# Performance work log

Hardware: AMD Instinct MI355X
Metric: run time of the kernel (lower is better)

Reference implementation:

```python
import jax, jax.numpy as jnp
import numpy as np

N = 50000
E = 800000
IN_C, HID_C, OUT_C = 256, 128, 64


def setup_inputs() -> dict:
    key = jax.random.key(0)
    k1, k2, k3, k4 = jax.random.split(key, 4)
    x = jax.random.normal(k1, (N, IN_C), dtype=jnp.float32)
    edge_index = jax.random.randint(k2, (2, E), 0, N, dtype=jnp.int64)
    # Glorot-ish init for GCN weights, zero bias (PyG default)
    W1 = jax.random.normal(k3, (IN_C, HID_C), dtype=jnp.float32) / np.sqrt(IN_C)
    b1 = jnp.zeros((HID_C,), dtype=jnp.float32)
    W2 = jax.random.normal(k4, (HID_C, OUT_C), dtype=jnp.float32) / np.sqrt(HID_C)
    b2 = jnp.zeros((OUT_C,), dtype=jnp.float32)
    return {"x": x, "edge_index": edge_index, "W1": W1, "b1": b1, "W2": W2, "b2": b2}


def _gcn_norm(edge_index, num_nodes):
    # Add self-loops, compute symmetric normalization D^-1/2 A D^-1/2 (PyG GCNConv default)
    loops = jnp.arange(num_nodes, dtype=edge_index.dtype)
    src = jnp.concatenate([edge_index[0], loops])  # message sources
    dst = jnp.concatenate([edge_index[1], loops])  # aggregation targets
    deg = jax.ops.segment_sum(jnp.ones_like(dst, dtype=jnp.float32), dst,
                              num_segments=num_nodes)
    dinv = jnp.where(deg > 0, jax.lax.rsqrt(deg), 0.0)
    norm = dinv[src] * dinv[dst]  # [E+N]
    return src, dst, norm


def _gcn_conv(x, W, b, src, dst, norm, num_nodes):
    h = x @ W                                   # [N, out]
    msg = h[src] * norm[:, None]                # gather + scale, [E+N, out]
    out = jax.ops.segment_sum(msg, dst, num_segments=num_nodes)  # scatter-add
    return out + b


def reference(x, edge_index, W1, b1, W2, b2):
    num_nodes = x.shape[0]
    src, dst, norm = _gcn_norm(edge_index, num_nodes)
    h = _gcn_conv(x, W1, b1, src, dst, norm, num_nodes)
    h = jax.nn.relu(h)
    # F.dropout(training=False) -> identity at inference
    return _gcn_conv(h, W2, b2, src, dst, norm, num_nodes)
```

## Files before the change

### kernel.cpp

```cpp
#include <hip/hip_runtime.h>
#include <hip/hip_bf16.h>


typedef __attribute__((ext_vector_type(8))) short short8;
typedef __attribute__((ext_vector_type(4))) float f32x4;

union BF8 {
    short8 s;
    uint4 u;
    __hip_bfloat162 h[4];
};

__device__ __forceinline__ unsigned short f32_to_bf16_rne(float f) {
    unsigned u = __float_as_uint(f);
    return (unsigned short)((u + 0x7fffu + ((u >> 16) & 1u)) >> 16);
}
__device__ __forceinline__ float bf_lo(unsigned v) { return __uint_as_float(v << 16); }
__device__ __forceinline__ float bf_hi(unsigned v) { return __uint_as_float(v & 0xffff0000u); }

__global__ void count_deg_kernel(const int* __restrict__ dst, int* __restrict__ counts, int e) {
    int i = blockIdx.x * blockDim.x + threadIdx.x;
    if (i < e) atomicAdd(&counts[dst[i]], 1);
}

__global__ void wfrag_zero_kernel(const float* __restrict__ W1, const float* __restrict__ W2,
                                  unsigned short* __restrict__ w1f,
                                  unsigned short* __restrict__ w2f,
                                  int* __restrict__ counts, int n) {
    int i = blockIdx.x * blockDim.x + threadIdx.x;
    if (i < n) counts[i] = 0;
    const float* W;
    unsigned short* WF;
    int KS, NCOL, idx;
    if (i < 32768) {
        W = W1; WF = w1f; KS = 8; NCOL = 128; idx = i;
    } else if (i < 32768 + 8192) {
        W = W2; WF = w2f; KS = 4; NCOL = 64; idx = i - 32768;
    } else return;
    int j = idx & 7;
    int lane = (idx >> 3) & 63;
    int f = idx >> 9;
    int ks = f % KS, nt = f / KS;
    int m16 = lane & 15, quad = lane >> 4;
    int ncol = nt * 16 + m16;
    int k = ks * 32 + quad * 8 + j;
    WF[idx] = f32_to_bf16_rne(W[k * NCOL + ncol]);
}

__global__ __launch_bounds__(256) void scan_partial_kernel(const int* __restrict__ counts,
                                                           int* __restrict__ bsums,
                                                           float* __restrict__ dinv, int n) {
    __shared__ int wsum[4];
    const int tid = threadIdx.x;
    const int lane = tid & 63, wv = tid >> 6;
    int base = blockIdx.x * 1024 + tid * 4;
    int s = 0;
#pragma unroll
    for (int j = 0; j < 4; j++) {
        int i = base + j;
        if (i < n) {
            int c = counts[i];
            s += c;
            dinv[i] = rsqrtf((float)c + 1.0f);
        }
    }
#pragma unroll
    for (int off = 1; off < 64; off <<= 1) {
        int y = __shfl_up(s, off, 64);
        if (lane >= off) s += y;
    }
    if (lane == 63) wsum[wv] = s;
    __syncthreads();
    if (tid == 0) bsums[blockIdx.x] = wsum[0] + wsum[1] + wsum[2] + wsum[3];
}

__global__ __launch_bounds__(256) void scan_final_kernel(const int* __restrict__ counts,
                                                         const int* __restrict__ bsums,
                                                         int* __restrict__ rowptr,
                                                         int* __restrict__ bcursor,
                                                         int n, int nb) {
    __shared__ int wsum[4];
    __shared__ int blockOff;
    const int tid = threadIdx.x;
    const int lane = tid & 63, wv = tid >> 6;
    if (tid < 64) {
        int v = (tid < nb) ? bsums[tid] : 0;
        int x = v;
#pragma unroll
        for (int off = 1; off < 64; off <<= 1) {
            int y = __shfl_up(x, off, 64);
            if (lane >= off) x += y;
        }
        int pref = (blockIdx.x == 0) ? 0 : __shfl(x, blockIdx.x - 1, 64);
        if (tid == 0) blockOff = pref;
    }
    int base = blockIdx.x * 1024 + tid * 4;
    int v[4];
#pragma unroll
    for (int j = 0; j < 4; j++) {
        int i = base + j;
        v[j] = (i < n) ? counts[i] : 0;
    }
    int tot = v[0] + v[1] + v[2] + v[3];
    int x = tot;
#pragma unroll
    for (int off = 1; off < 64; off <<= 1) {
        int y = __shfl_up(x, off, 64);
        if (lane >= off) x += y;
    }
    if (lane == 63) wsum[wv] = x;
    __syncthreads();
    int wpre = 0;
    for (int k = 0; k < wv; k++) wpre += wsum[k];
    int pre = blockOff + wpre + (x - tot);
#pragma unroll
    for (int j = 0; j < 4; j++) {
        int i = base + j;
        if (i <= n) rowptr[i] = pre;
        if (i < n && (i & 255) == 0) bcursor[i >> 8] = pre;
        pre += v[j];
    }
}

#define ACHUNK 2048
__global__ __launch_bounds__(256) void bucketA_kernel(const int* __restrict__ src,
                                                      const int* __restrict__ dst,
                                                      int* __restrict__ bcursor,
                                                      int2* __restrict__ tmp, int e, int nb) {
    __shared__ int sdst[ACHUNK];
    __shared__ int hist[256];
    const int tid = threadIdx.x;
    const int start = blockIdx.x * ACHUNK;
    const int cnt = min(ACHUNK, e - start);
    if (tid < nb) hist[tid] = 0;
    __syncthreads();
    for (int i = tid; i < cnt; i += 256) {
        int d = dst[start + i];
        sdst[i] = d;
        atomicAdd(&hist[d >> 8], 1);
    }
    __syncthreads();
    if (tid < nb) {
        int h = hist[tid];
        hist[tid] = (h > 0) ? atomicAdd(&bcursor[tid], h) : 0;
    }
    __syncthreads();
    for (int i = tid; i < cnt; i += 256) {
        int d = sdst[i];
        int slot = atomicAdd(&hist[d >> 8], 1);
        tmp[slot] = make_int2(src[start + i], d);
    }
}

__global__ __launch_bounds__(256) void bucketB_kernel(const int* __restrict__ rowptr,
                                                      const int2* __restrict__ tmp,
                                                      const float* __restrict__ dinv,
                                                      int2* __restrict__ sedge, int n) {
    __shared__ int lcur[256];
    __shared__ float ldinv[256];
    const int tid = threadIdx.x;
    const int nodeBase = blockIdx.x * 256;
    const int nNodes = min(256, n - nodeBase);
    if (tid < nNodes) {
        lcur[tid] = rowptr[nodeBase + tid];
        ldinv[tid] = dinv[nodeBase + tid];
    }
    __syncthreads();
    const int beg = rowptr[nodeBase];
    const int end = rowptr[nodeBase + nNodes];
    for (int i = beg + tid; i < end; i += 256) {
        int2 r = tmp[i];
        int j = r.y - nodeBase;
        float w = dinv[r.x] * ldinv[j];
        int pos = atomicAdd(&lcur[j], 1);
        sedge[pos] = make_int2(r.x, __float_as_int(w));
    }
}

__global__ __launch_bounds__(256) void agg128_kernel(
    const int* __restrict__ rowptr, const int2* __restrict__ sedge,
    const unsigned short* __restrict__ hb, const float* __restrict__ dinv,
    const float* __restrict__ bias, unsigned short* __restrict__ outb, int n) {
    int node = blockIdx.x * 8 + (threadIdx.x >> 5);
    if (node >= n) return;
    int sub = threadIdx.x & 31;
    float di = dinv[node];
    float d2 = di * di;
    uint2 sv = ((const uint2*)(hb + (size_t)node * 128))[sub];
    float a0 = d2 * bf_lo(sv.x), a1 = d2 * bf_hi(sv.x);
    float a2 = d2 * bf_lo(sv.y), a3 = d2 * bf_hi(sv.y);
    int beg = rowptr[node], end = rowptr[node + 1];
    int i = beg;
    for (; i + 8 <= end; i += 8) {
        int2 e[8];
        uint2 v[8];
#pragma unroll
        for (int j = 0; j < 8; j++) e[j] = sedge[i + j];
#pragma unroll
        for (int j = 0; j < 8; j++)
            v[j] = ((const uint2*)(hb + (size_t)e[j].x * 128))[sub];
#pragma unroll
        for (int j = 0; j < 8; j++) {
            float w = __int_as_float(e[j].y);
            a0 = fmaf(w, bf_lo(v[j].x), a0);
            a1 = fmaf(w, bf_hi(v[j].x), a1);
            a2 = fmaf(w, bf_lo(v[j].y), a2);
            a3 = fmaf(w, bf_hi(v[j].y), a3);
        }
    }
    for (; i + 4 <= end; i += 4) {
        int2 e[4];
        uint2 v[4];
#pragma unroll
        for (int j = 0; j < 4; j++) e[j] = sedge[i + j];
#pragma unroll
        for (int j = 0; j < 4; j++)
            v[j] = ((const uint2*)(hb + (size_t)e[j].x * 128))[sub];
#pragma unroll
        for (int j = 0; j < 4; j++) {
            float w = __int_as_float(e[j].y);
            a0 = fmaf(w, bf_lo(v[j].x), a0);
            a1 = fmaf(w, bf_hi(v[j].x), a1);
            a2 = fmaf(w, bf_lo(v[j].y), a2);
            a3 = fmaf(w, bf_hi(v[j].y), a3);
        }
    }
    for (; i < end; ++i) {
        int2 e = sedge[i];
        float w = __int_as_float(e.y);
        uint2 v = ((const uint2*)(hb + (size_t)e.x * 128))[sub];
        a0 = fmaf(w, bf_lo(v.x), a0);
        a1 = fmaf(w, bf_hi(v.x), a1);
        a2 = fmaf(w, bf_lo(v.y), a2);
        a3 = fmaf(w, bf_hi(v.y), a3);
    }
    float4 bv = ((const float4*)bias)[sub];
    float r0 = fmaxf(a0 + bv.x, 0.0f);
    float r1 = fmaxf(a1 + bv.y, 0.0f);
    float r2 = fmaxf(a2 + bv.z, 0.0f);
    float r3 = fmaxf(a3 + bv.w, 0.0f);
    BF8 p;
    p.h[0] = __float22bfloat162_rn(make_float2(r0, r1));
    p.h[1] = __float22bfloat162_rn(make_float2(r2, r3));
    ((uint2*)(outb + (size_t)node * 128))[sub] = make_uint2(p.u.x, p.u.y);
}

__global__ __launch_bounds__(256) void agg64_kernel(
    const int* __restrict__ rowptr, const int2* __restrict__ sedge,
    const unsigned short* __restrict__ hb, const float* __restrict__ dinv,
    const float* __restrict__ bias, float* __restrict__ out, int n) {
    int node = blockIdx.x * 8 + (threadIdx.x >> 5);
    if (node >= n) return;
    int sub = threadIdx.x & 31;
    float di = dinv[node];
    float d2 = di * di;
    unsigned sv = ((const unsigned*)(hb + (size_t)node * 64))[sub];
    float ax = d2 * bf_lo(sv), ay = d2 * bf_hi(sv);
    int beg = rowptr[node], end = rowptr[node + 1];
    int i = beg;
    for (; i + 8 <= end; i += 8) {
        int2 e[8];
        unsigned v[8];
#pragma unroll
        for (int j = 0; j < 8; j++) e[j] = sedge[i + j];
#pragma unroll
        for (int j = 0; j < 8; j++)
            v[j] = ((const unsigned*)(hb + (size_t)e[j].x * 64))[sub];
#pragma unroll
        for (int j = 0; j < 8; j++) {
            float w = __int_as_float(e[j].y);
            ax = fmaf(w, bf_lo(v[j]), ax);
            ay = fmaf(w, bf_hi(v[j]), ay);
        }
    }
    for (; i + 4 <= end; i += 4) {
        int2 e[4];
        unsigned v[4];
#pragma unroll
        for (int j = 0; j < 4; j++) e[j] = sedge[i + j];
#pragma unroll
        for (int j = 0; j < 4; j++)
            v[j] = ((const unsigned*)(hb + (size_t)e[j].x * 64))[sub];
#pragma unroll
        for (int j = 0; j < 4; j++) {
            float w = __int_as_float(e[j].y);
            ax = fmaf(w, bf_lo(v[j]), ax);
            ay = fmaf(w, bf_hi(v[j]), ay);
        }
    }
    for (; i < end; ++i) {
        int2 e = sedge[i];
        float w = __int_as_float(e.y);
        unsigned v = ((const unsigned*)(hb + (size_t)e.x * 64))[sub];
        ax = fmaf(w, bf_lo(v), ax);
        ay = fmaf(w, bf_hi(v), ay);
    }
    float2 bv = ((const float2*)bias)[sub];
    ((float2*)(out + (size_t)node * 64))[sub] = make_float2(ax + bv.x, ay + bv.y);
}

template <int NT, int KS, bool BFA>
__global__ __launch_bounds__(256) void mfma_gemm_kernel(
    const void* __restrict__ Av, const unsigned short* __restrict__ BFRAG,
    unsigned short* __restrict__ C, int M) {
    constexpr int NCOL = NT * 16;
    constexpr int K = KS * 32;
    constexpr int LSTRIDE = K + 8;
    __shared__ unsigned short Alds[64 * LSTRIDE];

    const int tid = threadIdx.x;
    const int wave = tid >> 6, lane = tid & 63;
    const int quad = lane >> 4, m16 = lane & 15;
    const int rowBase = blockIdx.x * 64;

    if constexpr (BFA) {
        const unsigned short* Ab = (const unsigned short*)Av;
        constexpr int ITERS = K / 32;
        uint4 v[ITERS];
#pragma unroll
        for (int it = 0; it < ITERS; it++) {
            int p = it * 2048 + tid * 8;
            int rg = rowBase + p / K;
            if (rg >= M) rg = M - 1;
            v[it] = *(const uint4*)(Ab + (size_t)rg * K + (p % K));
        }
#pragma unroll
        for (int it = 0; it < ITERS; it++) {
            int p = it * 2048 + tid * 8;
            *(uint4*)&Alds[(p / K) * LSTRIDE + (p % K)] = v[it];
        }
    } else {
        const float* Af = (const float*)Av;
        constexpr int HALVES = K / 128;
#pragma unroll
        for (int h = 0; h < HALVES; h++) {
            f32x4 v[8];
#pragma unroll
            for (int it = 0; it < 8; it++) {
                int p = (h * 8 + it) * 1024 + tid * 4;
                int rg = rowBase + p / K;
                if (rg >= M) rg = M - 1;
                v[it] = *(const f32x4*)(Af + (size_t)rg * K + (p % K));
            }
#pragma unroll
            for (int it = 0; it < 8; it++) {
                int p = (h * 8 + it) * 1024 + tid * 4;
                BF8 cv;
                cv.h[0] = __float22bfloat162_rn(make_float2(v[it].x, v[it].y));
                cv.h[1] = __float22bfloat162_rn(make_float2(v[it].z, v[it].w));
                *(uint2*)&Alds[(p / K) * LSTRIDE + (p % K)] = make_uint2(cv.u.x, cv.u.y);
            }
        }
    }
    __syncthreads();

    const unsigned short* Afrag0 = &Alds[(wave * 16 + m16) * LSTRIDE + quad * 8];
    const uint4* Bfrag = (const uint4*)BFRAG + lane;

    f32x4 acc[NT];
#pragma unroll
    for (int nt = 0; nt < NT; nt++) acc[nt] = f32x4{0.f, 0.f, 0.f, 0.f};

#pragma unroll
    for (int ks = 0; ks < KS; ks++) {
        BF8 af;
        af.u = *(const uint4*)(Afrag0 + ks * 32);
#pragma unroll
        for (int nt = 0; nt < NT; nt++) {
            BF8 bf;
            bf.u = Bfrag[(nt * KS + ks) * 64];
            acc[nt] = __builtin_amdgcn_mfma_f32_16x16x32_bf16(af.s, bf.s, acc[nt], 0, 0, 0);
        }
    }

    const int rowOut = rowBase + wave * 16 + quad * 4;
#pragma unroll
    for (int nt = 0; nt < NT; nt++) {
#pragma unroll
        for (int r = 0; r < 4; r++) {
            int row = rowOut + r;
            if (row < M)
                C[(size_t)row * NCOL + nt * 16 + m16] = f32_to_bf16_rne(acc[nt][r]);
        }
    }
}

extern "C" void kernel_launch(void* const* d_in, const int* in_sizes, int n_in,
                              void* d_out, int out_size, void* d_ws, size_t ws_size,
                              hipStream_t stream) {
    const float* x  = (const float*)d_in[0];
    const int*   ei = (const int*)d_in[1];
    const float* W1 = (const float*)d_in[2];
    const float* b1 = (const float*)d_in[3];
    const float* W2 = (const float*)d_in[4];
    const float* b2 = (const float*)d_in[5];
    float* out = (float*)d_out;

    const int IN_C = 256;
    const int N = in_sizes[0] / IN_C;
    const int E = in_sizes[1] / 2;
    const int* srcA = ei;
    const int* dstA = ei + E;

    char* ws = (char*)d_ws;
    const size_t KB = 1024, MB = 1024 * 1024;
    int*            counts  = (int*)(ws);
    float*          dinv    = (float*)(ws + 256 * KB);
    int*            rowptr  = (int*)(ws + 512 * KB);
    int*            bcursor = (int*)(ws + 768 * KB);
    int*            bsums   = (int*)(ws + 992 * KB);
    unsigned short* w1f     = (unsigned short*)(ws + 1 * MB);
    unsigned short* w2f     = (unsigned short*)(ws + 1 * MB + 64 * KB);
    int2*           sedge   = (int2*)(ws + 2 * MB);
    int2*           tmp     = (int2*)(ws + 9 * MB);
    unsigned short* h1b     = (unsigned short*)(ws + 16 * MB);
    unsigned short* a1b     = (unsigned short*)(ws + 29 * MB);
    unsigned short* h2b     = h1b;

    const int eb256 = (E + 255) / 256;
    const int nbScan = (N + 1 + 1023) / 1024;
    const int NB = (N + 255) / 256;
    const int gGemm = (N + 63) / 64;
    const int gWfrag = (max(N, 32768 + 8192) + 255) / 256;

    wfrag_zero_kernel<<<gWfrag, 256, 0, stream>>>(W1, W2, w1f, w2f, counts, N);
    count_deg_kernel<<<eb256, 256, 0, stream>>>(dstA, counts, E);
    scan_partial_kernel<<<nbScan, 256, 0, stream>>>(counts, bsums, dinv, N);
    scan_final_kernel<<<nbScan, 256, 0, stream>>>(counts, bsums, rowptr, bcursor, N, nbScan);
    bucketA_kernel<<<(E + ACHUNK - 1) / ACHUNK, 256, 0, stream>>>(srcA, dstA, bcursor, tmp, E, NB);
    bucketB_kernel<<<NB, 256, 0, stream>>>(rowptr, tmp, dinv, sedge, N);

    mfma_gemm_kernel<8, 8, false><<<gGemm, 256, 0, stream>>>(x, w1f, h1b, N);
    agg128_kernel<<<(N + 7) / 8, 256, 0, stream>>>(rowptr, sedge, h1b, dinv, b1, a1b, N);

    mfma_gemm_kernel<4, 4, true><<<gGemm, 256, 0, stream>>>(a1b, w2f, h2b, N);
    agg64_kernel<<<(N + 7) / 8, 256, 0, stream>>>(rowptr, sedge, h2b, dinv, b2, out, N);
}
```

Before: 243.2 us.

## Fuse scan passes with decoupled lookback, merge GEMM1 with bucketing, widen aggregation loads

The two-pass prefix scan becomes a single kernel in which each block publishes its sum with a flag and then spin-waits on earlier blocks' flags. The first GEMM and the edge-bucketing pass now share one launch, with blocks split by index, so independent work runs concurrently and two launches are removed. The aggregation kernels now use 16 lanes per node with wider 16-byte (128-wide layer) or 8-byte (64-wide layer) loads, handling twice as many nodes per block. The spin-wait assumes all earlier scan blocks are resident, which holds for the small grid here, and the fused kernel's shared-memory footprint is the GEMM's size.

```diff
diff --git a/kernel.cpp b/kernel.cpp
--- a/kernel.cpp
+++ b/kernel.cpp
@@ -26,9 +26,10 @@
 __global__ void wfrag_zero_kernel(const float* __restrict__ W1, const float* __restrict__ W2,
                                   unsigned short* __restrict__ w1f,
                                   unsigned short* __restrict__ w2f,
-                                  int* __restrict__ counts, int n) {
+                                  int* __restrict__ counts, int* __restrict__ bflag, int n) {
     int i = blockIdx.x * blockDim.x + threadIdx.x;
     if (i < n) counts[i] = 0;
+    if (i < 64) bflag[i] = 0;
     const float* W;
     unsigned short* WF;
     int KS, NCOL, idx;
@@ -47,59 +48,27 @@
     WF[idx] = f32_to_bf16_rne(W[k * NCOL + ncol]);
 }
 
-__global__ __launch_bounds__(256) void scan_partial_kernel(const int* __restrict__ counts,
-                                                           int* __restrict__ bsums,
-                                                           float* __restrict__ dinv, int n) {
+__global__ __launch_bounds__(256) void scan_fused_kernel(const int* __restrict__ counts,
+                                                         float* __restrict__ dinv,
+                                                         int* __restrict__ rowptr,
+                                                         int* __restrict__ bcursor,
+                                                         int* __restrict__ bsum,
+                                                         int* __restrict__ bflag, int n) {
     __shared__ int wsum[4];
+    __shared__ int blockOff;
     const int tid = threadIdx.x;
     const int lane = tid & 63, wv = tid >> 6;
-    int base = blockIdx.x * 1024 + tid * 4;
-    int s = 0;
+    const int bid = blockIdx.x;
+    int base = bid * 1024 + tid * 4;
+    int v[4];
 #pragma unroll
     for (int j = 0; j < 4; j++) {
         int i = base + j;
         if (i < n) {
             int c = counts[i];
-            s += c;
+            v[j] = c;
             dinv[i] = rsqrtf((float)c + 1.0f);
-        }
-    }
-#pragma unroll
-    for (int off = 1; off < 64; off <<= 1) {
-        int y = __shfl_up(s, off, 64);
-        if (lane >= off) s += y;
-    }
-    if (lane == 63) wsum[wv] = s;
-    __syncthreads();
-    if (tid == 0) bsums[blockIdx.x] = wsum[0] + wsum[1] + wsum[2] + wsum[3];
-}
-
-__global__ __launch_bounds__(256) void scan_final_kernel(const int* __restrict__ counts,
-                                                         const int* __restrict__ bsums,
-                                                         int* __restrict__ rowptr,
-                                                         int* __restrict__ bcursor,
-                                                         int n, int nb) {
-    __shared__ int wsum[4];
-    __shared__ int blockOff;
-    const int tid = threadIdx.x;
-    const int lane = tid & 63, wv = tid >> 6;
-    if (tid < 64) {
-        int v = (tid < nb) ? bsums[tid] : 0;
-        int x = v;
-#pragma unroll
-        for (int off = 1; off < 64; off <<= 1) {
-            int y = __shfl_up(x, off, 64);
-            if (lane >= off) x += y;
-        }
-        int pref = (blockIdx.x == 0) ? 0 : __shfl(x, blockIdx.x - 1, 64);
-        if (tid == 0) blockOff = pref;
-    }
-    int base = blockIdx.x * 1024 + tid * 4;
-    int v[4];
-#pragma unroll
-    for (int j = 0; j < 4; j++) {
-        int i = base + j;
-        v[j] = (i < n) ? counts[i] : 0;
+        } else v[j] = 0;
     }
     int tot = v[0] + v[1] + v[2] + v[3];
     int x = tot;
@@ -112,6 +81,23 @@
     __syncthreads();
     int wpre = 0;
     for (int k = 0; k < wv; k++) wpre += wsum[k];
+    if (tid == 0) {
+        bsum[bid] = wsum[0] + wsum[1] + wsum[2] + wsum[3];
+        __threadfence();
+        atomicExch(&bflag[bid], 1);
+    }
+    if (wv == 0) {
+        int p = 0;
+        if (lane < bid) {
+            while (atomicAdd(&bflag[lane], 0) == 0) {}
+            __threadfence();
+            p = atomicAdd(&bsum[lane], 0);
+        }
+#pragma unroll
+        for (int off = 1; off < 64; off <<= 1) p += __shfl_xor(p, off, 64);
+        if (lane == 0) blockOff = p;
+    }
+    __syncthreads();
     int pre = blockOff + wpre + (x - tot);
 #pragma unroll
     for (int j = 0; j < 4; j++) {
@@ -123,32 +109,96 @@
 }
 
 #define ACHUNK 2048
-__global__ __launch_bounds__(256) void bucketA_kernel(const int* __restrict__ src,
-                                                      const int* __restrict__ dst,
-                                                      int* __restrict__ bcursor,
-                                                      int2* __restrict__ tmp, int e, int nb) {
-    __shared__ int sdst[ACHUNK];
-    __shared__ int hist[256];
+__global__ __launch_bounds__(256) void gemm1_bucketA_kernel(
+    const float* __restrict__ A, const unsigned short* __restrict__ BFRAG,
+    unsigned short* __restrict__ C, int M, int gGemm,
+    const int* __restrict__ src, const int* __restrict__ dst,
+    int* __restrict__ bcursor, int2* __restrict__ tmp, int e, int nb) {
+    constexpr int NT = 8, KS = 8;
+    constexpr int K = KS * 32;
+    constexpr int LSTRIDE = K + 8;
+    __shared__ char smem[64 * LSTRIDE * 2];
+
     const int tid = threadIdx.x;
-    const int start = blockIdx.x * ACHUNK;
-    const int cnt = min(ACHUNK, e - start);
-    if (tid < nb) hist[tid] = 0;
-    __syncthreads();
-    for (int i = tid; i < cnt; i += 256) {
-        int d = dst[start + i];
-        sdst[i] = d;
-        atomicAdd(&hist[d >> 8], 1);
-    }
-    __syncthreads();
-    if (tid < nb) {
-        int h = hist[tid];
-        hist[tid] = (h > 0) ? atomicAdd(&bcursor[tid], h) : 0;
-    }
-    __syncthreads();
-    for (int i = tid; i < cnt; i += 256) {
-        int d = sdst[i];
-        int slot = atomicAdd(&hist[d >> 8], 1);
-        tmp[slot] = make_int2(src[start + i], d);
+    if ((int)blockIdx.x < gGemm) {
+        unsigned short* Alds = (unsigned short*)smem;
+        const int wave = tid >> 6, lane = tid & 63;
+        const int quad = lane >> 4, m16 = lane & 15;
+        const int rowBase = blockIdx.x * 64;
+
+        constexpr int HALVES = K / 128;
+#pragma unroll
+        for (int h = 0; h < HALVES; h++) {
+            f32x4 v[8];
+#pragma unroll
+            for (int it = 0; it < 8; it++) {
+                int p = (h * 8 + it) * 1024 + tid * 4;
+                int rg = rowBase + p / K;
+                if (rg >= M) rg = M - 1;
+                v[it] = *(const f32x4*)(A + (size_t)rg * K + (p % K));
+            }
+#pragma unroll
+            for (int it = 0; it < 8; it++) {
+                int p = (h * 8 + it) * 1024 + tid * 4;
+                BF8 cv;
+                cv.h[0] = __float22bfloat162_rn(make_float2(v[it].x, v[it].y));
+                cv.h[1] = __float22bfloat162_rn(make_float2(v[it].z, v[it].w));
+                *(uint2*)&Alds[(p / K) * LSTRIDE + (p % K)] = make_uint2(cv.u.x, cv.u.y);
+            }
+        }
+        __syncthreads();
+
+        const unsigned short* Afrag0 = &Alds[(wave * 16 + m16) * LSTRIDE + quad * 8];
+        const uint4* Bfrag = (const uint4*)BFRAG + lane;
+
+        f32x4 acc[NT];
+#pragma unroll
+        for (int nt = 0; nt < NT; nt++) acc[nt] = f32x4{0.f, 0.f, 0.f, 0.f};
+#pragma unroll
+        for (int ks = 0; ks < KS; ks++) {
+            BF8 af;
+            af.u = *(const uint4*)(Afrag0 + ks * 32);
+#pragma unroll
+            for (int nt = 0; nt < NT; nt++) {
+                BF8 bf;
+                bf.u = Bfrag[(nt * KS + ks) * 64];
+                acc[nt] = __builtin_amdgcn_mfma_f32_16x16x32_bf16(af.s, bf.s, acc[nt], 0, 0, 0);
+            }
+        }
+        const int rowOut = rowBase + wave * 16 + quad * 4;
+#pragma unroll
+        for (int nt = 0; nt < NT; nt++) {
+#pragma unroll
+            for (int r = 0; r < 4; r++) {
+                int row = rowOut + r;
+                if (row < M)
+                    C[(size_t)row * 128 + nt * 16 + m16] = f32_to_bf16_rne(acc[nt][r]);
+            }
+        }
+    } else {
+        int* sdst = (int*)smem;
+        int* hist = (int*)(smem + 8192);
+        const int b0 = blockIdx.x - gGemm;
+        const int start = b0 * ACHUNK;
+        const int cnt = min(ACHUNK, e - start);
+        if (tid < nb) hist[tid] = 0;
+        __syncthreads();
+        for (int i = tid; i < cnt; i += 256) {
+            int d = dst[start + i];
+            sdst[i] = d;
+            atomicAdd(&hist[d >> 8], 1);
+        }
+        __syncthreads();
+        if (tid < nb) {
+            int h = hist[tid];
+            hist[tid] = (h > 0) ? atomicAdd(&bcursor[tid], h) : 0;
+        }
+        __syncthreads();
+        for (int i = tid; i < cnt; i += 256) {
+            int d = sdst[i];
+            int slot = atomicAdd(&hist[d >> 8], 1);
+            tmp[slot] = make_int2(src[start + i], d);
+        }
     }
 }
 
@@ -181,12 +231,64 @@
     const int* __restrict__ rowptr, const int2* __restrict__ sedge,
     const unsigned short* __restrict__ hb, const float* __restrict__ dinv,
     const float* __restrict__ bias, unsigned short* __restrict__ outb, int n) {
-    int node = blockIdx.x * 8 + (threadIdx.x >> 5);
+    int node = blockIdx.x * 16 + (threadIdx.x >> 4);
     if (node >= n) return;
-    int sub = threadIdx.x & 31;
+    int sub = threadIdx.x & 15;
     float di = dinv[node];
     float d2 = di * di;
-    uint2 sv = ((const uint2*)(hb + (size_t)node * 128))[sub];
+    uint4 sv = ((const uint4*)(hb + (size_t)node * 128))[sub];
+    float a0 = d2 * bf_lo(sv.x), a1 = d2 * bf_hi(sv.x);
+    float a2 = d2 * bf_lo(sv.y), a3 = d2 * bf_hi(sv.y);
+    float a4 = d2 * bf_lo(sv.z), a5 = d2 * bf_hi(sv.z);
+    float a6 = d2 * bf_lo(sv.w), a7 = d2 * bf_hi(sv.w);
+    int beg = rowptr[node], end = rowptr[node + 1];
+    int i = beg;
+    for (; i + 4 <= end; i += 4) {
+        int2 e[4];
+        uint4 v[4];
+#pragma unroll
+        for (int j = 0; j < 4; j++) e[j] = sedge[i + j];
+#pragma unroll
+        for (int j = 0; j < 4; j++)
+            v[j] = ((const uint4*)(hb + (size_t)e[j].x * 128))[sub];
+#pragma unroll
+        for (int j = 0; j < 4; j++) {
+            float w = __int_as_float(e[j].y);
+            a0 = fmaf(w, bf_lo(v[j].x), a0); a1 = fmaf(w, bf_hi(v[j].x), a1);
+            a2 = fmaf(w, bf_lo(v[j].y), a2); a3 = fmaf(w, bf_hi(v[j].y), a3);
+            a4 = fmaf(w, bf_lo(v[j].z), a4); a5 = fmaf(w, bf_hi(v[j].z), a5);
+            a6 = fmaf(w, bf_lo(v[j].w), a6); a7 = fmaf(w, bf_hi(v[j].w), a7);
+        }
+    }
+    for (; i < end; ++i) {
+        int2 e = sedge[i];
+        float w = __int_as_float(e.y);
+        uint4 v = ((const uint4*)(hb + (size_t)e.x * 128))[sub];
+        a0 = fmaf(w, bf_lo(v.x), a0); a1 = fmaf(w, bf_hi(v.x), a1);
+        a2 = fmaf(w, bf_lo(v.y), a2); a3 = fmaf(w, bf_hi(v.y), a3);
+        a4 = fmaf(w, bf_lo(v.z), a4); a5 = fmaf(w, bf_hi(v.z), a5);
+        a6 = fmaf(w, bf_lo(v.w), a6); a7 = fmaf(w, bf_hi(v.w), a7);
+    }
+    float4 b0 = ((const float4*)bias)[sub * 2];
+    float4 b1 = ((const float4*)bias)[sub * 2 + 1];
+    BF8 p;
+    p.h[0] = __float22bfloat162_rn(make_float2(fmaxf(a0 + b0.x, 0.f), fmaxf(a1 + b0.y, 0.f)));
+    p.h[1] = __float22bfloat162_rn(make_float2(fmaxf(a2 + b0.z, 0.f), fmaxf(a3 + b0.w, 0.f)));
+    p.h[2] = __float22bfloat162_rn(make_float2(fmaxf(a4 + b1.x, 0.f), fmaxf(a5 + b1.y, 0.f)));
+    p.h[3] = __float22bfloat162_rn(make_float2(fmaxf(a6 + b1.z, 0.f), fmaxf(a7 + b1.w, 0.f)));
+    ((uint4*)(outb + (size_t)node * 128))[sub] = p.u;
+}
+
+__global__ __launch_bounds__(256) void agg64_kernel(
+    const int* __restrict__ rowptr, const int2* __restrict__ sedge,
+    const unsigned short* __restrict__ hb, const float* __restrict__ dinv,
+    const float* __restrict__ bias, float* __restrict__ out, int n) {
+    int node = blockIdx.x * 16 + (threadIdx.x >> 4);
+    if (node >= n) return;
+    int sub = threadIdx.x & 15;
+    float di = dinv[node];
+    float d2 = di * di;
+    uint2 sv = ((const uint2*)(hb + (size_t)node * 64))[sub];
     float a0 = d2 * bf_lo(sv.x), a1 = d2 * bf_hi(sv.x);
     float a2 = d2 * bf_lo(sv.y), a3 = d2 * bf_hi(sv.y);
     int beg = rowptr[node], end = rowptr[node + 1];
@@ -198,14 +300,12 @@
         for (int j = 0; j < 8; j++) e[j] = sedge[i + j];
 #pragma unroll
         for (int j = 0; j < 8; j++)
-            v[j] = ((const uint2*)(hb + (size_t)e[j].x * 128))[sub];
+            v[j] = ((const uint2*)(hb + (size_t)e[j].x * 64))[sub];
 #pragma unroll
         for (int j = 0; j < 8; j++) {
             float w = __int_as_float(e[j].y);
-            a0 = fmaf(w, bf_lo(v[j].x), a0);
-            a1 = fmaf(w, bf_hi(v[j].x), a1);
-            a2 = fmaf(w, bf_lo(v[j].y), a2);
-            a3 = fmaf(w, bf_hi(v[j].y), a3);
+            a0 = fmaf(w, bf_lo(v[j].x), a0); a1 = fmaf(w, bf_hi(v[j].x), a1);
+            a2 = fmaf(w, bf_lo(v[j].y), a2); a3 = fmaf(w, bf_hi(v[j].y), a3);
         }
     }
     for (; i + 4 <= end; i += 4) {
@@ -215,93 +315,29 @@
         for (int j = 0; j < 4; j++) e[j] = sedge[i + j];
 #pragma unroll
         for (int j = 0; j < 4; j++)
-            v[j] = ((const uint2*)(hb + (size_t)e[j].x * 128))[sub];
+            v[j] = ((const uint2*)(hb + (size_t)e[j].x * 64))[sub];
 #pragma unroll
         for (int j = 0; j < 4; j++) {
             float w = __int_as_float(e[j].y);
-            a0 = fmaf(w, bf_lo(v[j].x), a0);
-            a1 = fmaf(w, bf_hi(v[j].x), a1);
-            a2 = fmaf(w, bf_lo(v[j].y), a2);
-            a3 = fmaf(w, bf_hi(v[j].y), a3);
+            a0 = fmaf(w, bf_lo(v[j].x), a0); a1 = fmaf(w, bf_hi(v[j].x), a1);
+            a2 = fmaf(w, bf_lo(v[j].y), a2); a3 = fmaf(w, bf_hi(v[j].y), a3);
         }
     }
     for (; i < end; ++i) {
         int2 e = sedge[i];
         float w = __int_as_float(e.y);
-        uint2 v = ((const uint2*)(hb + (size_t)e.x * 128))[sub];
-        a0 = fmaf(w, bf_lo(v.x), a0);
-        a1 = fmaf(w, bf_hi(v.x), a1);
-        a2 = fmaf(w, bf_lo(v.y), a2);
-        a3 = fmaf(w, bf_hi(v.y), a3);
+        uint2 v = ((const uint2*)(hb + (size_t)e.x * 64))[sub];
+        a0 = fmaf(w, bf_lo(v.x), a0); a1 = fmaf(w, bf_hi(v.x), a1);
+        a2 = fmaf(w, bf_lo(v.y), a2); a3 = fmaf(w, bf_hi(v.y), a3);
     }
     float4 bv = ((const float4*)bias)[sub];
-    float r0 = fmaxf(a0 + bv.x, 0.0f);
-    float r1 = fmaxf(a1 + bv.y, 0.0f);
-    float r2 = fmaxf(a2 + bv.z, 0.0f);
-    float r3 = fmaxf(a3 + bv.w, 0.0f);
-    BF8 p;
-    p.h[0] = __float22bfloat162_rn(make_float2(r0, r1));
-    p.h[1] = __float22bfloat162_rn(make_float2(r2, r3));
-    ((uint2*)(outb + (size_t)node * 128))[sub] = make_uint2(p.u.x, p.u.y);
-}
-
-__global__ __launch_bounds__(256) void agg64_kernel(
-    const int* __restrict__ rowptr, const int2* __restrict__ sedge,
-    const unsigned short* __restrict__ hb, const float* __restrict__ dinv,
-    const float* __restrict__ bias, float* __restrict__ out, int n) {
-    int node = blockIdx.x * 8 + (threadIdx.x >> 5);
-    if (node >= n) return;
-    int sub = threadIdx.x & 31;
-    float di = dinv[node];
-    float d2 = di * di;
-    unsigned sv = ((const unsigned*)(hb + (size_t)node * 64))[sub];
-    float ax = d2 * bf_lo(sv), ay = d2 * bf_hi(sv);
-    int beg = rowptr[node], end = rowptr[node + 1];
-    int i = beg;
-    for (; i + 8 <= end; i += 8) {
-        int2 e[8];
-        unsigned v[8];
-#pragma unroll
-        for (int j = 0; j < 8; j++) e[j] = sedge[i + j];
-#pragma unroll
-        for (int j = 0; j < 8; j++)
-            v[j] = ((const unsigned*)(hb + (size_t)e[j].x * 64))[sub];
-#pragma unroll
-        for (int j = 0; j < 8; j++) {
-            float w = __int_as_float(e[j].y);
-            ax = fmaf(w, bf_lo(v[j]), ax);
-            ay = fmaf(w, bf_hi(v[j]), ay);
-        }
-    }
-    for (; i + 4 <= end; i += 4) {
-        int2 e[4];
-        unsigned v[4];
-#pragma unroll
-        for (int j = 0; j < 4; j++) e[j] = sedge[i + j];
-#pragma unroll
-        for (int j = 0; j < 4; j++)
-            v[j] = ((const unsigned*)(hb + (size_t)e[j].x * 64))[sub];
-#pragma unroll
-        for (int j = 0; j < 4; j++) {
-            float w = __int_as_float(e[j].y);
-            ax = fmaf(w, bf_lo(v[j]), ax);
-            ay = fmaf(w, bf_hi(v[j]), ay);
-        }
-    }
-    for (; i < end; ++i) {
-        int2 e = sedge[i];
-        float w = __int_as_float(e.y);
-        unsigned v = ((const unsigned*)(hb + (size_t)e.x * 64))[sub];
-        ax = fmaf(w, bf_lo(v), ax);
-        ay = fmaf(w, bf_hi(v), ay);
-    }
-    float2 bv = ((const float2*)bias)[sub];
-    ((float2*)(out + (size_t)node * 64))[sub] = make_float2(ax + bv.x, ay + bv.y);
-}
-
-template <int NT, int KS, bool BFA>
-__global__ __launch_bounds__(256) void mfma_gemm_kernel(
-    const void* __restrict__ Av, const unsigned short* __restrict__ BFRAG,
+    ((float4*)(out + (size_t)node * 64))[sub] =
+        make_float4(a0 + bv.x, a1 + bv.y, a2 + bv.z, a3 + bv.w);
+}
+
+template <int NT, int KS>
+__global__ __launch_bounds__(256) void mfma_gemm_bfA_kernel(
+    const unsigned short* __restrict__ A, const unsigned short* __restrict__ BFRAG,
     unsigned short* __restrict__ C, int M) {
     constexpr int NCOL = NT * 16;
     constexpr int K = KS * 32;
@@ -313,44 +349,19 @@
     const int quad = lane >> 4, m16 = lane & 15;
     const int rowBase = blockIdx.x * 64;
 
-    if constexpr (BFA) {
-        const unsigned short* Ab = (const unsigned short*)Av;
-        constexpr int ITERS = K / 32;
-        uint4 v[ITERS];
-#pragma unroll
-        for (int it = 0; it < ITERS; it++) {
-            int p = it * 2048 + tid * 8;
-            int rg = rowBase + p / K;
-            if (rg >= M) rg = M - 1;
-            v[it] = *(const uint4*)(Ab + (size_t)rg * K + (p % K));
-        }
-#pragma unroll
-        for (int it = 0; it < ITERS; it++) {
-            int p = it * 2048 + tid * 8;
-            *(uint4*)&Alds[(p / K) * LSTRIDE + (p % K)] = v[it];
-        }
-    } else {
-        const float* Af = (const float*)Av;
-        constexpr int HALVES = K / 128;
-#pragma unroll
-        for (int h = 0; h < HALVES; h++) {
-            f32x4 v[8];
-#pragma unroll
-            for (int it = 0; it < 8; it++) {
-                int p = (h * 8 + it) * 1024 + tid * 4;
-                int rg = rowBase + p / K;
-                if (rg >= M) rg = M - 1;
-                v[it] = *(const f32x4*)(Af + (size_t)rg * K + (p % K));
-            }
-#pragma unroll
-            for (int it = 0; it < 8; it++) {
-                int p = (h * 8 + it) * 1024 + tid * 4;
-                BF8 cv;
-                cv.h[0] = __float22bfloat162_rn(make_float2(v[it].x, v[it].y));
-                cv.h[1] = __float22bfloat162_rn(make_float2(v[it].z, v[it].w));
-                *(uint2*)&Alds[(p / K) * LSTRIDE + (p % K)] = make_uint2(cv.u.x, cv.u.y);
-            }
-        }
+    constexpr int ITERS = K / 32;
+    uint4 v[ITERS];
+#pragma unroll
+    for (int it = 0; it < ITERS; it++) {
+        int p = it * 2048 + tid * 8;
+        int rg = rowBase + p / K;
+        if (rg >= M) rg = M - 1;
+        v[it] = *(const uint4*)(A + (size_t)rg * K + (p % K));
+    }
+#pragma unroll
+    for (int it = 0; it < ITERS; it++) {
+        int p = it * 2048 + tid * 8;
+        *(uint4*)&Alds[(p / K) * LSTRIDE + (p % K)] = v[it];
     }
     __syncthreads();
 
@@ -360,7 +371,6 @@
     f32x4 acc[NT];
 #pragma unroll
     for (int nt = 0; nt < NT; nt++) acc[nt] = f32x4{0.f, 0.f, 0.f, 0.f};
-
 #pragma unroll
     for (int ks = 0; ks < KS; ks++) {
         BF8 af;
@@ -372,7 +382,6 @@
             acc[nt] = __builtin_amdgcn_mfma_f32_16x16x32_bf16(af.s, bf.s, acc[nt], 0, 0, 0);
         }
     }
-
     const int rowOut = rowBase + wave * 16 + quad * 4;
 #pragma unroll
     for (int nt = 0; nt < NT; nt++) {
@@ -408,7 +417,8 @@
     float*          dinv    = (float*)(ws + 256 * KB);
     int*            rowptr  = (int*)(ws + 512 * KB);
     int*            bcursor = (int*)(ws + 768 * KB);
-    int*            bsums   = (int*)(ws + 992 * KB);
+    int*            bflag   = (int*)(ws + 960 * KB);
+    int*            bsum    = (int*)(ws + 992 * KB);
     unsigned short* w1f     = (unsigned short*)(ws + 1 * MB);
     unsigned short* w2f     = (unsigned short*)(ws + 1 * MB + 64 * KB);
     int2*           sedge   = (int2*)(ws + 2 * MB);
@@ -421,18 +431,16 @@
     const int nbScan = (N + 1 + 1023) / 1024;
     const int NB = (N + 255) / 256;
     const int gGemm = (N + 63) / 64;
+    const int nbA = (E + ACHUNK - 1) / ACHUNK;
     const int gWfrag = (max(N, 32768 + 8192) + 255) / 256;
 
-    wfrag_zero_kernel<<<gWfrag, 256, 0, stream>>>(W1, W2, w1f, w2f, counts, N);
+    wfrag_zero_kernel<<<gWfrag, 256, 0, stream>>>(W1, W2, w1f, w2f, counts, bflag, N);
     count_deg_kernel<<<eb256, 256, 0, stream>>>(dstA, counts, E);
-    scan_partial_kernel<<<nbScan, 256, 0, stream>>>(counts, bsums, dinv, N);
-    scan_final_kernel<<<nbScan, 256, 0, stream>>>(counts, bsums, rowptr, bcursor, N, nbScan);
-    bucketA_kernel<<<(E + ACHUNK - 1) / ACHUNK, 256, 0, stream>>>(srcA, dstA, bcursor, tmp, E, NB);
+    scan_fused_kernel<<<nbScan, 256, 0, stream>>>(counts, dinv, rowptr, bcursor, bsum, bflag, N);
+    gemm1_bucketA_kernel<<<gGemm + nbA, 256, 0, stream>>>(
+        x, w1f, h1b, N, gGemm, srcA, dstA, bcursor, tmp, E, NB);
     bucketB_kernel<<<NB, 256, 0, stream>>>(rowptr, tmp, dinv, sedge, N);
-
-    mfma_gemm_kernel<8, 8, false><<<gGemm, 256, 0, stream>>>(x, w1f, h1b, N);
-    agg128_kernel<<<(N + 7) / 8, 256, 0, stream>>>(rowptr, sedge, h1b, dinv, b1, a1b, N);
-
-    mfma_gemm_kernel<4, 4, true><<<gGemm, 256, 0, stream>>>(a1b, w2f, h2b, N);
-    agg64_kernel<<<(N + 7) / 8, 256, 0, stream>>>(rowptr, sedge, h2b, dinv, b2, out, N);
-}
+    agg128_kernel<<<(N + 15) / 16, 256, 0, stream>>>(rowptr, sedge, h1b, dinv, b1, a1b, N);
+    mfma_gemm_bfA_kernel<4, 4><<<gGemm, 256, 0, stream>>>(a1b, w2f, h2b, N);
+    agg64_kernel<<<(N + 15) / 16, 256, 0, stream>>>(rowptr, sedge, h2b, dinv, b2, out, N);
+}
```

Result: faster. 227.8 us (-6.3%).
